# Kernel optimization log

Measured on AMD Instinct MI355X. Metric: run time of the kernel, lower is better.

## Reference

```python
import jax, jax.numpy as jnp
import numpy as np

B, M, NT, V, D, H, E, S = 4, 12, 12, 10000, 64, 3, 512, 32


def setup_inputs() -> dict:
    key = jax.random.key(0)
    ks = jax.random.split(key, 16)
    def rn(k, shape, scale=0.05):
        return jax.random.normal(k, shape, dtype=jnp.float32) * scale
    return {
        "tendency": jax.random.normal(ks[0], (B, M, V), dtype=jnp.float32),
        "periodicity": jax.random.normal(ks[1], (B, NT, V), dtype=jnp.float32),
        "edges": jax.random.randint(ks[2], (H, E, S), 0, V),
        "w1": rn(ks[3], (1, D)), "b1": rn(ks[4], (D,)),
        "w2": rn(ks[5], (D, D)), "b2": rn(ks[6], (D,)),
        "attn_w": rn(ks[7], (D, D)), "attn_a": rn(ks[8], (2 * D, 1)),
        "w_ih": rn(ks[9], (4 * D, D)), "w_hh": rn(ks[10], (4 * D, D)),
        "b_ih": rn(ks[11], (4 * D,)), "b_hh": rn(ks[12], (4 * D,)),
        "w_out": rn(ks[13], (2 * D, 1)), "b_out": rn(ks[14], (1,)),
    }


def _hypersage(X, edges, w, b):
    # X: (N, V, F); edges: (E, S) node indices. All edges have size S <= Q,
    # so torch's random subsampling is the identity.
    n, v, f = X.shape
    e, s = edges.shape
    gathered = X[:, edges, :]                      # (N, E, S, F)
    agg = gathered.mean(axis=2)                    # (N, E, F)
    flat = edges.reshape(-1)                       # (E*S,)
    contrib = jnp.broadcast_to(agg[:, :, None, :], (n, e, s, f)).reshape(n, e * s, f)
    X_out = jnp.zeros((n, v, f), X.dtype).at[:, flat, :].add(contrib)
    deg = jnp.zeros((v,), X.dtype).at[flat].add(1.0)
    deg = jnp.maximum(deg, 1.0)
    X_out = X_out / deg[None, :, None]
    return X_out @ w + b                           # Linear fc


def _attention(Xs, attn_w, attn_a):
    # Xs: (H, N, V, D)
    ref = Xs.mean(axis=0)                          # (N, V, D)
    wx = Xs @ attn_w                               # (H, N, V, D)
    wr = ref @ attn_w                              # (N, V, D)
    z = jnp.concatenate([wx, jnp.broadcast_to(wr[None], wx.shape)], axis=-1) @ attn_a
    z = jax.nn.leaky_relu(z, negative_slope=0.2)   # (H, N, V, 1)
    alpha = jax.nn.softmax(z, axis=0)
    return (alpha * Xs).sum(axis=0)                # (N, V, D)


def _lstm_final(x, w_ih, w_hh, b_ih, b_hh):
    # x: (BV, T, D) -> final hidden state (BV, D). PyTorch gate order i,f,g,o.
    bv, t, d = x.shape
    xg = x @ w_ih.T + (b_ih + b_hh)                # precompute input gates (BV, T, 4D)
    def step(carry, xg_t):
        h, c = carry
        g = xg_t + h @ w_hh.T
        i, f, gg, o = jnp.split(g, 4, axis=-1)
        c = jax.nn.sigmoid(f) * c + jax.nn.sigmoid(i) * jnp.tanh(gg)
        h = jax.nn.sigmoid(o) * jnp.tanh(c)
        return (h, c), None
    h0 = jnp.zeros((bv, d), x.dtype)
    (h, _), _ = jax.lax.scan(step, (h0, h0), jnp.swapaxes(xg, 0, 1))
    return h


def _branch(seq, edges, w1, b1, w2, b2, attn_w, attn_a, w_ih, w_hh, b_ih, b_hh):
    b, t, v = seq.shape
    X = seq.reshape(b * t, v, 1)                   # fold time into batch (same DAMHG per step)
    def per_hg(e):
        return _hypersage(_hypersage(X, e, w1, b1), e, w2, b2)
    xs = jax.vmap(per_hg)(edges)                   # (H, B*T, V, D)
    fused = _attention(xs, attn_w, attn_a)         # (B*T, V, D)
    d = fused.shape[-1]
    seq_v = fused.reshape(b, t, v, d).transpose(0, 2, 1, 3).reshape(b * v, t, d)
    h = _lstm_final(seq_v, w_ih, w_hh, b_ih, b_hh)
    return h.reshape(b, v, d)


def reference(tendency, periodicity, edges, w1, b1, w2, b2, attn_w, attn_a, w_ih, w_hh, b_ih, b_hh, w_out, b_out):
    h_t = _branch(tendency, edges, w1, b1, w2, b2, attn_w, attn_a, w_ih, w_hh, b_ih, b_hh)
    h_p = _branch(periodicity, edges, w1, b1, w2, b2, attn_w, attn_a, w_ih, w_hh, b_ih, b_hh)
    fusion = jnp.concatenate([h_t, h_p], axis=-1)  # (B, V, 2D)
    out = fusion @ w_out + b_out                   # (B, V, 1)
    return out[..., 0]
```

## Files before the change

### kernel.cpp

```cpp
#include <hip/hip_runtime.h>

#define NV 10000
#define NB 4
#define NTT 12
#define NSEQ 48
#define NH 3
#define NE 512
#define NS 32
#define ND 64
#define NVT 313

#define S_U   0
#define S_C1  64
#define S_V1  128
#define S_V2  192
#define S_SC  256
#define S_GU  272
#define S_GC  528
#define S_G0  784
#define F_INV 1040
#define F_M   (F_INV + NH*NV)
#define F_PQ  (F_M + NH*NV)
#define F_HT  (F_PQ + 4*NV*NSEQ)
#define I_CNT (F_HT + 2*NB*NV)
#define I_CUR (I_CNT + NH*NV)
#define I_OFF (I_CUR + NH*NV)
#define I_SLOT (I_OFF + NH*NV)
#define F_DYN (I_SLOT + NH*NE*NS)
#define XT_SZ  (NV*NSEQ)
#define AGG_SZ (NH*NE*NSEQ)
#define YZ_SZ  (NH*NV*NSEQ)

#define NZERO (2*NH*NV + NB*NV)

typedef __attribute__((ext_vector_type(8))) _Float16 f16x8;
typedef __attribute__((ext_vector_type(4))) float f32x4;

__device__ __forceinline__ unsigned short f2h(float x) {
  union { _Float16 h; unsigned short u; } c;
  c.h = (_Float16)x;
  return c.u;
}
__device__ __forceinline__ f16x8 ldsH(const unsigned short* p) {
  union { uint4 u; f16x8 v; } x;
  x.u = *(const uint4*)p;
  return x.v;
}

__global__ void k_init(const float* __restrict__ w1, const float* __restrict__ b1,
                       const float* __restrict__ w2, const float* __restrict__ b2,
                       const float* __restrict__ attn_w, const float* __restrict__ attn_a,
                       const float* __restrict__ w_ih, const float* __restrict__ b_ih,
                       const float* __restrict__ b_hh, float* __restrict__ ws,
                       int* __restrict__ cnt, float* __restrict__ out) {
  const int tid = threadIdx.x;
  if (blockIdx.x != 0) {
    const int g = (blockIdx.x - 1) * 256 + tid;
    if (g < 2 * NH * NV) cnt[g] = 0;
    else if (g < NZERO) out[g - 2 * NH * NV] = 0.0f;
    return;
  }
  __shared__ float u_s[64], c1_s[64];
  if (tid < 64) {
    float v1 = 0.f, v2 = 0.f, u = 0.f, c1 = 0.f;
    for (int d = 0; d < 64; ++d) {
      const float aw = attn_w[tid * 64 + d];
      v1 += aw * attn_a[d];
      v2 += aw * attn_a[64 + d];
      const float w2v = w2[d * 64 + tid];
      u  += w1[d] * w2v;
      c1 += b1[d] * w2v;
    }
    ws[S_U + tid] = u;  ws[S_C1 + tid] = c1;
    ws[S_V1 + tid] = v1; ws[S_V2 + tid] = v2;
    u_s[tid] = u; c1_s[tid] = c1;
  }
  __syncthreads();
  if (tid == 0) {
    float al = 0.f, be = 0.f, ga = 0.f, de = 0.f, ep = 0.f;
    for (int d = 0; d < 64; ++d) {
      const float v1 = ws[S_V1 + d], v2 = ws[S_V2 + d];
      al += u_s[d] * v1;  be += c1_s[d] * v1;
      ga += u_s[d] * v2;  de += c1_s[d] * v2;
      ep += b2[d] * (v1 + v2);
    }
    ws[S_SC + 0] = al; ws[S_SC + 1] = be; ws[S_SC + 2] = ga;
    ws[S_SC + 3] = de; ws[S_SC + 4] = ep;
  }
  {
    const int j = tid;
    float gu = 0.f, gc = 0.f, g0 = 0.f;
    for (int d = 0; d < 64; ++d) {
      const float w = w_ih[j * 64 + d];
      gu += w * u_s[d]; gc += w * c1_s[d]; g0 += w * b2[d];
    }
    ws[S_GU + j] = gu; ws[S_GC + j] = gc;
    ws[S_G0 + j] = g0 + b_ih[j] + b_hh[j];
  }
}

__global__ void k_count(const int* __restrict__ edges, int* __restrict__ counts) {
  const int g = blockIdx.x * 256 + threadIdx.x;
  if (g >= NH * NE * NS) return;
  const int h = g >> 14;
  atomicAdd(&counts[h * NV + edges[g]], 1);
}

__global__ void k_scan(const int* __restrict__ counts, int* __restrict__ offs,
                       float* __restrict__ invdeg, float* __restrict__ mvec) {
  const int h = blockIdx.x;
  const int tid = threadIdx.x;
  const int base = h * NV;
  const int CH = 10;
  int local[10];
  int run = 0;
  for (int i = 0; i < CH; ++i) {
    const int v = tid * CH + i;
    const int c = (v < NV) ? counts[base + v] : 0;
    local[i] = run; run += c;
  }
  __shared__ int sd[1024];
  sd[tid] = run;
  __syncthreads();
  int acc = run;
  for (int off = 1; off < 1024; off <<= 1) {
    const int t = (tid >= off) ? sd[tid - off] : 0;
    __syncthreads();
    acc += t; sd[tid] = acc;
    __syncthreads();
  }
  const int excl = acc - run;
  for (int i = 0; i < CH; ++i) {
    const int v = tid * CH + i;
    if (v < NV) {
      offs[base + v] = excl + local[i];
      const int c = counts[base + v];
      invdeg[base + v] = 1.0f / (float)((c > 0) ? c : 1);
      mvec[base + v] = (c > 0) ? 1.0f : 0.0f;
    }
  }
}

__global__ void k_fill(const int* __restrict__ edges, const int* __restrict__ offs,
                       int* __restrict__ cursor, int* __restrict__ slot_edge) {
  const int g = blockIdx.x * 256 + threadIdx.x;
  if (g >= NH * NE * NS) return;
  const int h = g >> 14;
  const int e = (g >> 5) & (NE - 1);
  const int v = edges[g];
  const int pos = atomicAdd(&cursor[h * NV + v], 1);
  slot_edge[h * NE * NS + offs[h * NV + v] + pos] = e;
}

__global__ void k_trans2(const float* __restrict__ s0, const float* __restrict__ s1,
                         float* __restrict__ xT, int xtS) {
  __shared__ float tile[128][49];
  const float* seq = blockIdx.y ? s1 : s0;
  float* o = xT + (size_t)blockIdx.y * xtS;
  const int v0 = blockIdx.x * 128;
  const int tid = threadIdx.x;
  for (int i = tid; i < 128 * NSEQ; i += 256) {
    const int n = i / 128, vl = i % 128;
    const int v = v0 + vl;
    tile[vl][n] = (v < NV) ? seq[n * NV + v] : 0.0f;
  }
  __syncthreads();
  for (int i = tid; i < 128 * NSEQ; i += 256) {
    const int vl = i / NSEQ, n = i % NSEQ;
    const int v = v0 + vl;
    if (v < NV) o[v * NSEQ + n] = tile[vl][n];
  }
}

__global__ void k_eagg1(const int* __restrict__ edges, const float* __restrict__ xT,
                        int xtS, float* __restrict__ agg, int aggS) {
  const int g = blockIdx.x * 256 + threadIdx.x;
  if (g >= NH * NE * 12 * 8) return;
  const float* x = xT + (size_t)blockIdx.y * xtS;
  float* a = agg + (size_t)blockIdx.y * aggS;
  const int sub = g & 7;
  const int o = g >> 3;
  const int n0 = (o % 12) * 4;
  const int e = (o / 12) % NE;
  const int h = o / (12 * NE);
  const int* ep = edges + (h * NE + e) * NS + sub * 4;
  float4 acc = make_float4(0.f, 0.f, 0.f, 0.f);
  #pragma unroll
  for (int s = 0; s < 4; ++s) {
    const float4 t = *(const float4*)&x[ep[s] * NSEQ + n0];
    acc.x += t.x; acc.y += t.y; acc.z += t.z; acc.w += t.w;
  }
  #pragma unroll
  for (int m = 1; m < 8; m <<= 1) {
    acc.x += __shfl_xor(acc.x, m);
    acc.y += __shfl_xor(acc.y, m);
    acc.z += __shfl_xor(acc.z, m);
    acc.w += __shfl_xor(acc.w, m);
  }
  if (sub == 0) {
    acc.x *= (1.0f / NS); acc.y *= (1.0f / NS); acc.z *= (1.0f / NS); acc.w *= (1.0f / NS);
    *(float4*)&a[(h * NE + e) * NSEQ + n0] = acc;
  }
}

__global__ void k_eagg2(const int* __restrict__ edges, const float* __restrict__ ysum,
                        int yS, const float* __restrict__ invdeg,
                        float* __restrict__ agg, int aggS) {
  const int g = blockIdx.x * 256 + threadIdx.x;
  if (g >= NH * NE * 12 * 8) return;
  const float* y = ysum + (size_t)blockIdx.y * yS;
  float* a = agg + (size_t)blockIdx.y * aggS;
  const int sub = g & 7;
  const int o = g >> 3;
  const int n0 = (o % 12) * 4;
  const int e = (o / 12) % NE;
  const int h = o / (12 * NE);
  const int* ep = edges + (h * NE + e) * NS + sub * 4;
  float4 acc = make_float4(0.f, 0.f, 0.f, 0.f);
  #pragma unroll
  for (int s = 0; s < 4; ++s) {
    const int v = ep[s];
    const float iv = invdeg[h * NV + v];
    const float4 t = *(const float4*)&y[(h * NV + v) * NSEQ + n0];
    acc.x += t.x * iv; acc.y += t.y * iv; acc.z += t.z * iv; acc.w += t.w * iv;
  }
  #pragma unroll
  for (int m = 1; m < 8; m <<= 1) {
    acc.x += __shfl_xor(acc.x, m);
    acc.y += __shfl_xor(acc.y, m);
    acc.z += __shfl_xor(acc.z, m);
    acc.w += __shfl_xor(acc.w, m);
  }
  if (sub == 0) {
    acc.x *= (1.0f / NS); acc.y *= (1.0f / NS); acc.z *= (1.0f / NS); acc.w *= (1.0f / NS);
    *(float4*)&a[(h * NE + e) * NSEQ + n0] = acc;
  }
}

__global__ void k_vg(const int* __restrict__ counts, const int* __restrict__ offs,
                     const int* __restrict__ slot_edge, const float* __restrict__ agg,
                     int aggS, float* __restrict__ outv, int outS) {
  const int g = blockIdx.x * 256 + threadIdx.x;
  if (g >= NH * NV * 12) return;
  const float* a = agg + (size_t)blockIdx.y * aggS;
  float* o = outv + (size_t)blockIdx.y * outS;
  const int n0 = (g % 12) * 4;
  const int v = (g / 12) % NV;
  const int h = g / (12 * NV);
  const int beg = offs[h * NV + v];
  const int cnt = counts[h * NV + v];
  const int* se = slot_edge + h * NE * NS;
  float4 acc = make_float4(0.f, 0.f, 0.f, 0.f);
  for (int i = 0; i < cnt; ++i) {
    const int e = se[beg + i];
    const float4 t = *(const float4*)&a[(h * NE + e) * NSEQ + n0];
    acc.x += t.x; acc.y += t.y; acc.z += t.z; acc.w += t.w;
  }
  *(float4*)&o[(h * NV + v) * NSEQ + n0] = acc;
}

__global__ void k_vgattn(const int* __restrict__ counts, const int* __restrict__ offs,
                         const int* __restrict__ slot_edge, const float* __restrict__ agg,
                         int aggS, const float* __restrict__ invdeg,
                         const float* __restrict__ mvec, const float* __restrict__ ws,
                         unsigned int* __restrict__ pq, int br0) {
  const int g = blockIdx.x * 256 + threadIdx.x;
  if (g >= NV * 12) return;
  const int bi = blockIdx.y;
  const float* a = agg + (size_t)bi * aggS;
  unsigned int* pbuf = pq + (size_t)(bi + br0) * NV * NSEQ;
  const int n0 = (g % 12) * 4;
  const int v = g / 12;
  const float al = ws[S_SC + 0], be = ws[S_SC + 1], ga = ws[S_SC + 2],
              de = ws[S_SC + 3], ep = ws[S_SC + 4];
  union { float4 v4; float f[4]; } zh[3];
  float mh[3];
  #pragma unroll
  for (int h = 0; h < NH; ++h) {
    const int beg = offs[h * NV + v];
    const int cnt = counts[h * NV + v];
    const int* se = slot_edge + h * NE * NS;
    float4 acc = make_float4(0.f, 0.f, 0.f, 0.f);
    for (int i = 0; i < cnt; ++i) {
      const int e = se[beg + i];
      const float4 t = *(const float4*)&a[(h * NE + e) * NSEQ + n0];
      acc.x += t.x; acc.y += t.y; acc.z += t.z; acc.w += t.w;
    }
    const float iv = invdeg[h * NV + v];
    zh[h].v4 = make_float4(acc.x * iv, acc.y * iv, acc.z * iv, acc.w * iv);
    mh[h] = mvec[h * NV + v];
  }
  const float mb = (mh[0] + mh[1] + mh[2]) * (1.f / 3.f);
  uint4 o4;
  unsigned int* op = (unsigned int*)&o4;
  #pragma unroll
  for (int j = 0; j < 4; ++j) {
    const float z0 = zh[0].f[j], z1 = zh[1].f[j], z2 = zh[2].f[j];
    const float zb = (z0 + z1 + z2) * (1.f / 3.f);
    float sc[3];
    const float zt[3] = {z0, z1, z2};
    #pragma unroll
    for (int h = 0; h < NH; ++h) {
      const float s = al * zt[h] + be * mh[h] + ga * zb + de * mb + ep;
      sc[h] = (s > 0.f) ? s : 0.2f * s;
    }
    const float mx = fmaxf(sc[0], fmaxf(sc[1], sc[2]));
    const float e0 = __expf(sc[0] - mx), e1 = __expf(sc[1] - mx), e2 = __expf(sc[2] - mx);
    const float inv = 1.0f / (e0 + e1 + e2);
    const float pv = (e0 * z0 + e1 * z1 + e2 * z2) * inv;
    const float qv = (e0 * mh[0] + e1 * mh[1] + e2 * mh[2]) * inv;
    op[j] = (unsigned int)f2h(pv) | ((unsigned int)f2h(qv) << 16);
  }
  *(uint4*)&pbuf[v * NSEQ + n0] = o4;
}

#define RS2 72
__launch_bounds__(256, 4)
__global__ void k_lstm2(const float* __restrict__ w_hh, const float* __restrict__ ws,
                        const unsigned int* __restrict__ pqbase,
                        const float* __restrict__ w_out, const float* __restrict__ b_out,
                        float* __restrict__ out) {
  __shared__ __align__(16) unsigned short smem[2 * 32 * RS2];
  __shared__ unsigned int pq_sh[NTT][32];
  const int tid = threadIdx.x;
  const int w = tid >> 6, lane = tid & 63, q = lane >> 4, l15 = lane & 15;
  const int bid = blockIdx.x;
  const int vt = bid % NVT;
  const int b  = (bid / NVT) % NB;
  const int br = bid / (NVT * NB);
  const int v0 = vt * 32;
  const int d = w * 16 + l15;

  union HU { uint4 u; f16x8 v; };

  const unsigned int* pqb = pqbase + (size_t)br * NV * NSEQ;
  if (tid < 96) {
    const int s = tid / 3, f4 = tid % 3;
    const int v = v0 + s;
    uint4 val = make_uint4(0u, 0u, 0u, 0u);
    if (v < NV) val = *(const uint4*)&pqb[v * NSEQ + b * NTT + f4 * 4];
    pq_sh[f4 * 4 + 0][s] = val.x; pq_sh[f4 * 4 + 1][s] = val.y;
    pq_sh[f4 * 4 + 2][s] = val.z; pq_sh[f4 * 4 + 3][s] = val.w;
  }

  f16x8 Bf[4][2];
  #pragma unroll
  for (int g = 0; g < 4; ++g)
    #pragma unroll
    for (int kh = 0; kh < 2; ++kh) {
      const float* wp = w_hh + (g * 64 + d) * 64 + kh * 32 + q * 8;
      const float4 lo = *(const float4*)wp;
      const float4 hi = *(const float4*)(wp + 4);
      HU f;
      f.u.x = (unsigned int)f2h(lo.x) | ((unsigned int)f2h(lo.y) << 16);
      f.u.y = (unsigned int)f2h(lo.z) | ((unsigned int)f2h(lo.w) << 16);
      f.u.z = (unsigned int)f2h(hi.x) | ((unsigned int)f2h(hi.y) << 16);
      f.u.w = (unsigned int)f2h(hi.z) | ((unsigned int)f2h(hi.w) << 16);
      Bf[g][kh] = f.v;
    }

  HU bex[4];
  #pragma unroll
  for (int g = 0; g < 4; ++g) {
    const float gu = ws[S_GU + g * 64 + d];
    const float gc = ws[S_GC + g * 64 + d];
    const float g0 = ws[S_G0 + g * 64 + d];
    bex[g].u.x = (q == 0) ? ((unsigned int)f2h(gu) | ((unsigned int)f2h(gc) << 16)) : 0u;
    bex[g].u.y = (q == 0) ? (unsigned int)f2h(g0) : 0u;
    bex[g].u.z = 0u; bex[g].u.w = 0u;
  }
  const float WO = w_out[br * 64 + d];
  const float BO = b_out[0];
  __syncthreads();

  f32x4 cst[2];
  float pr[2][4];
  #pragma unroll
  for (int mi = 0; mi < 2; ++mi) cst[mi] = (f32x4){0.f, 0.f, 0.f, 0.f};
  const f32x4 z4 = (f32x4){0.f, 0.f, 0.f, 0.f};

  #pragma unroll 1
  for (int t = 0; t < NTT; ++t) {
    const unsigned short* hr = smem + ((t + 1) & 1) * (32 * RS2);
    unsigned short* hw = smem + (t & 1) * (32 * RS2);
    const bool last = (t == NTT - 1);
    #pragma unroll
    for (int mi = 0; mi < 2; ++mi) {
      HU ae;
      ae.u.x = (q == 0) ? pq_sh[t][mi * 16 + l15] : 0u;
      ae.u.y = (q == 0) ? 0x3C00u : 0u;
      ae.u.z = 0u; ae.u.w = 0u;
      f32x4 aI = __builtin_amdgcn_mfma_f32_16x16x32_f16(ae.v, bex[0].v, z4, 0, 0, 0);
      f32x4 aF = __builtin_amdgcn_mfma_f32_16x16x32_f16(ae.v, bex[1].v, z4, 0, 0, 0);
      f32x4 aG = __builtin_amdgcn_mfma_f32_16x16x32_f16(ae.v, bex[2].v, z4, 0, 0, 0);
      f32x4 aO = __builtin_amdgcn_mfma_f32_16x16x32_f16(ae.v, bex[3].v, z4, 0, 0, 0);
      if (t > 0) {
        #pragma unroll
        for (int kh = 0; kh < 2; ++kh) {
          const f16x8 Ah = ldsH(&hr[(mi * 16 + l15) * RS2 + kh * 32 + q * 8]);
          aI = __builtin_amdgcn_mfma_f32_16x16x32_f16(Ah, Bf[0][kh], aI, 0, 0, 0);
          aF = __builtin_amdgcn_mfma_f32_16x16x32_f16(Ah, Bf[1][kh], aF, 0, 0, 0);
          aG = __builtin_amdgcn_mfma_f32_16x16x32_f16(Ah, Bf[2][kh], aG, 0, 0, 0);
          aO = __builtin_amdgcn_mfma_f32_16x16x32_f16(Ah, Bf[3][kh], aO, 0, 0, 0);
        }
      }
      #pragma unroll
      for (int r = 0; r < 4; ++r) {
        const float c  = cst[mi][r];
        const float ea = __expf(-aI[r]);
        const float eb = __expf(-2.0f * aG[r]);
        const float ef = __expf(-aF[r]);
        const float A  = 1.0f + ea, Bb = 1.0f + eb, Fd = 1.0f + ef;
        const float P  = A * Bb;
        const float numer = fmaf(c, P, (1.0f - eb) * Fd);
        const float cn = numer * __builtin_amdgcn_rcpf(Fd * P);
        cst[mi][r] = cn;
        const float ec = __expf(-aO[r]);
        const float ed = __expf(-2.0f * cn);
        const float h = (1.0f - ed) *
            __builtin_amdgcn_rcpf((1.0f + ec) * (1.0f + ed));
        if (!last) {
          hw[(mi * 16 + q * 4 + r) * RS2 + d] = f2h(h);
        } else {
          pr[mi][r] = h * WO;
        }
      }
    }
    __syncthreads();
  }
  float* fbuf = (float*)smem;
  #pragma unroll
  for (int mi = 0; mi < 2; ++mi)
    #pragma unroll
    for (int r = 0; r < 4; ++r) {
      float v = pr[mi][r];
      v += __shfl_xor(v, 1);
      v += __shfl_xor(v, 2);
      v += __shfl_xor(v, 4);
      v += __shfl_xor(v, 8);
      if (l15 == 0) fbuf[w * 32 + mi * 16 + q * 4 + r] = v;
    }
  __syncthreads();
  if (tid < 32) {
    const int v = v0 + tid;
    if (v < NV) {
      const float s = fbuf[tid] + fbuf[32 + tid] + fbuf[64 + tid] + fbuf[96 + tid];
      atomicAdd(&out[b * NV + v], s + ((br == 0) ? BO : 0.0f));
    }
  }
}

extern "C" void kernel_launch(void* const* d_in, const int* in_sizes, int n_in,
                              void* d_out, int out_size, void* d_ws, size_t ws_size,
                              hipStream_t stream) {
  const float* tend   = (const float*)d_in[0];
  const float* peri   = (const float*)d_in[1];
  const int*   edges  = (const int*)d_in[2];
  const float* w1     = (const float*)d_in[3];
  const float* b1     = (const float*)d_in[4];
  const float* w2     = (const float*)d_in[5];
  const float* b2     = (const float*)d_in[6];
  const float* attn_w = (const float*)d_in[7];
  const float* attn_a = (const float*)d_in[8];
  const float* w_ih   = (const float*)d_in[9];
  const float* w_hh   = (const float*)d_in[10];
  const float* b_ih   = (const float*)d_in[11];
  const float* b_hh   = (const float*)d_in[12];
  const float* w_out  = (const float*)d_in[13];
  const float* b_out  = (const float*)d_in[14];
  float* out = (float*)d_out;
  float* ws  = (float*)d_ws;
  int*   iws = (int*)d_ws;
  int* cnt = iws + I_CNT;
  int* cur = iws + I_CUR;
  int* off = iws + I_OFF;
  int* sed = iws + I_SLOT;
  unsigned int* pqw = (unsigned int*)(ws + F_PQ);

  const size_t need2 = ((size_t)F_DYN + 2 * (XT_SZ + AGG_SZ + YZ_SZ)) * 4;
  const bool batched = ws_size >= need2;
  const int nb = batched ? 2 : 1;
  float* XT  = ws + F_DYN;
  float* AGG = XT + (size_t)nb * XT_SZ;
  float* YZ  = AGG + (size_t)nb * AGG_SZ;

  k_init<<<1 + (NZERO + 255) / 256, 256, 0, stream>>>(
      w1, b1, w2, b2, attn_w, attn_a, w_ih, b_ih, b_hh, ws, cnt, out);
  k_count<<<(NH * NE * NS) / 256, 256, 0, stream>>>(edges, cnt);
  k_scan<<<NH, 1024, 0, stream>>>(cnt, off, ws + F_INV, ws + F_M);
  k_fill<<<(NH * NE * NS) / 256, 256, 0, stream>>>(edges, off, cur, sed);

  const int g_eagg = (NH * NE * 12 * 8) / 256;
  const int g_vg   = (NH * NV * 12 + 255) / 256;
  const int g_attn = (NV * 12 + 255) / 256;
  if (batched) {
    k_trans2<<<dim3((NV + 127) / 128, 2), 256, 0, stream>>>(tend, peri, XT, XT_SZ);
    k_eagg1<<<dim3(g_eagg, 2), 256, 0, stream>>>(edges, XT, XT_SZ, AGG, AGG_SZ);
    k_vg<<<dim3(g_vg, 2), 256, 0, stream>>>(cnt, off, sed, AGG, AGG_SZ, YZ, YZ_SZ);
    k_eagg2<<<dim3(g_eagg, 2), 256, 0, stream>>>(edges, YZ, YZ_SZ, ws + F_INV, AGG, AGG_SZ);
    k_vgattn<<<dim3(g_attn, 2), 256, 0, stream>>>(cnt, off, sed, AGG, AGG_SZ,
                                                  ws + F_INV, ws + F_M, ws, pqw, 0);
  } else {
    for (int br = 0; br < 2; ++br) {
      const float* seq = br ? peri : tend;
      k_trans2<<<dim3((NV + 127) / 128, 1), 256, 0, stream>>>(seq, seq, XT, 0);
      k_eagg1<<<dim3(g_eagg, 1), 256, 0, stream>>>(edges, XT, 0, AGG, 0);
      k_vg<<<dim3(g_vg, 1), 256, 0, stream>>>(cnt, off, sed, AGG, 0, YZ, 0);
      k_eagg2<<<dim3(g_eagg, 1), 256, 0, stream>>>(edges, YZ, 0, ws + F_INV, AGG, 0);
      k_vgattn<<<dim3(g_attn, 1), 256, 0, stream>>>(cnt, off, sed, AGG, 0,
                                                    ws + F_INV, ws + F_M, ws, pqw, br);
    }
  }
  k_lstm2<<<NVT * NB * 2, 256, 0, stream>>>(w_hh, ws, pqw, w_out, b_out, out);
}
```

Measured before the change: 238.1 us.

## Fold transpose into init kernel, fuse fill into scan, prescale tanh gate weights

Merges the input transpose into the init kernel's grid and moves the CSR slot fill into the scan kernel after a barrier. Together these remove two kernel launches from the preprocessing chain. The g-gate weights and biases of the LSTM are prescaled by -2 so the tanh exponent needs no per-step multiply. The LSTM launch bounds are raised to 8 blocks per CU. Doing the fill inside the scan runs it with only 3 blocks, which lowers parallelism, and the tighter launch bounds may cause register spills.

```diff
diff --git a/kernel.cpp b/kernel.cpp
--- a/kernel.cpp
+++ b/kernel.cpp
@@ -32,6 +32,8 @@
 #define YZ_SZ  (NH*NV*NSEQ)
 
 #define NZERO (2*NH*NV + NB*NV)
+#define ZBLK  ((NZERO + 255) / 256)
+#define TRB   ((NV + 127) / 128)
 
 typedef __attribute__((ext_vector_type(8))) _Float16 f16x8;
 typedef __attribute__((ext_vector_type(4))) float f32x4;
@@ -52,8 +54,30 @@
                        const float* __restrict__ attn_w, const float* __restrict__ attn_a,
                        const float* __restrict__ w_ih, const float* __restrict__ b_ih,
                        const float* __restrict__ b_hh, float* __restrict__ ws,
-                       int* __restrict__ cnt, float* __restrict__ out) {
+                       int* __restrict__ cnt, float* __restrict__ out,
+                       const float* __restrict__ s0, const float* __restrict__ s1,
+                       float* __restrict__ xT, int xtS) {
   const int tid = threadIdx.x;
+  if (blockIdx.x > ZBLK) {
+    __shared__ float tile[128][49];
+    const int bx = blockIdx.x - 1 - ZBLK;
+    const int brn = bx / TRB;
+    const int v0 = (bx % TRB) * 128;
+    const float* seq = brn ? s1 : s0;
+    float* o = xT + (size_t)brn * xtS;
+    for (int i = tid; i < 128 * NSEQ; i += 256) {
+      const int n = i / 128, vl = i % 128;
+      const int v = v0 + vl;
+      tile[vl][n] = (v < NV) ? seq[n * NV + v] : 0.0f;
+    }
+    __syncthreads();
+    for (int i = tid; i < 128 * NSEQ; i += 256) {
+      const int vl = i / NSEQ, n = i % NSEQ;
+      const int v = v0 + vl;
+      if (v < NV) o[v * NSEQ + n] = tile[vl][n];
+    }
+    return;
+  }
   if (blockIdx.x != 0) {
     const int g = (blockIdx.x - 1) * 256 + tid;
     if (g < 2 * NH * NV) cnt[g] = 0;
@@ -106,7 +130,9 @@
   atomicAdd(&counts[h * NV + edges[g]], 1);
 }
 
-__global__ void k_scan(const int* __restrict__ counts, int* __restrict__ offs,
+__global__ void k_scan(const int* __restrict__ edges, const int* __restrict__ counts,
+                       int* __restrict__ offs, int* __restrict__ cursor,
+                       int* __restrict__ slot_edge,
                        float* __restrict__ invdeg, float* __restrict__ mvec) {
   const int h = blockIdx.x;
   const int tid = threadIdx.x;
@@ -139,36 +165,12 @@
       mvec[base + v] = (c > 0) ? 1.0f : 0.0f;
     }
   }
-}
-
-__global__ void k_fill(const int* __restrict__ edges, const int* __restrict__ offs,
-                       int* __restrict__ cursor, int* __restrict__ slot_edge) {
-  const int g = blockIdx.x * 256 + threadIdx.x;
-  if (g >= NH * NE * NS) return;
-  const int h = g >> 14;
-  const int e = (g >> 5) & (NE - 1);
-  const int v = edges[g];
-  const int pos = atomicAdd(&cursor[h * NV + v], 1);
-  slot_edge[h * NE * NS + offs[h * NV + v] + pos] = e;
-}
-
-__global__ void k_trans2(const float* __restrict__ s0, const float* __restrict__ s1,
-                         float* __restrict__ xT, int xtS) {
-  __shared__ float tile[128][49];
-  const float* seq = blockIdx.y ? s1 : s0;
-  float* o = xT + (size_t)blockIdx.y * xtS;
-  const int v0 = blockIdx.x * 128;
-  const int tid = threadIdx.x;
-  for (int i = tid; i < 128 * NSEQ; i += 256) {
-    const int n = i / 128, vl = i % 128;
-    const int v = v0 + vl;
-    tile[vl][n] = (v < NV) ? seq[n * NV + v] : 0.0f;
-  }
   __syncthreads();
-  for (int i = tid; i < 128 * NSEQ; i += 256) {
-    const int vl = i / NSEQ, n = i % NSEQ;
-    const int v = v0 + vl;
-    if (v < NV) o[v * NSEQ + n] = tile[vl][n];
+  const int be = h * NE * NS;
+  for (int i = tid; i < NE * NS; i += 1024) {
+    const int v = edges[be + i];
+    const int pos = atomicAdd(&cursor[base + v], 1);
+    slot_edge[be + offs[base + v] + pos] = i >> 5;
   }
 }
 
@@ -315,7 +317,7 @@
 }
 
 #define RS2 72
-__launch_bounds__(256, 4)
+__launch_bounds__(256, 8)
 __global__ void k_lstm2(const float* __restrict__ w_hh, const float* __restrict__ ws,
                         const unsigned int* __restrict__ pqbase,
                         const float* __restrict__ w_out, const float* __restrict__ b_out,
@@ -345,26 +347,29 @@
 
   f16x8 Bf[4][2];
   #pragma unroll
-  for (int g = 0; g < 4; ++g)
+  for (int g = 0; g < 4; ++g) {
+    const float sc = (g == 2) ? -2.0f : 1.0f;
     #pragma unroll
     for (int kh = 0; kh < 2; ++kh) {
       const float* wp = w_hh + (g * 64 + d) * 64 + kh * 32 + q * 8;
       const float4 lo = *(const float4*)wp;
       const float4 hi = *(const float4*)(wp + 4);
       HU f;
-      f.u.x = (unsigned int)f2h(lo.x) | ((unsigned int)f2h(lo.y) << 16);
-      f.u.y = (unsigned int)f2h(lo.z) | ((unsigned int)f2h(lo.w) << 16);
-      f.u.z = (unsigned int)f2h(hi.x) | ((unsigned int)f2h(hi.y) << 16);
-      f.u.w = (unsigned int)f2h(hi.z) | ((unsigned int)f2h(hi.w) << 16);
+      f.u.x = (unsigned int)f2h(sc * lo.x) | ((unsigned int)f2h(sc * lo.y) << 16);
+      f.u.y = (unsigned int)f2h(sc * lo.z) | ((unsigned int)f2h(sc * lo.w) << 16);
+      f.u.z = (unsigned int)f2h(sc * hi.x) | ((unsigned int)f2h(sc * hi.y) << 16);
+      f.u.w = (unsigned int)f2h(sc * hi.z) | ((unsigned int)f2h(sc * hi.w) << 16);
       Bf[g][kh] = f.v;
     }
+  }
 
   HU bex[4];
   #pragma unroll
   for (int g = 0; g < 4; ++g) {
-    const float gu = ws[S_GU + g * 64 + d];
-    const float gc = ws[S_GC + g * 64 + d];
-    const float g0 = ws[S_G0 + g * 64 + d];
+    const float sc = (g == 2) ? -2.0f : 1.0f;
+    const float gu = sc * ws[S_GU + g * 64 + d];
+    const float gc = sc * ws[S_GC + g * 64 + d];
+    const float g0 = sc * ws[S_G0 + g * 64 + d];
     bex[g].u.x = (q == 0) ? ((unsigned int)f2h(gu) | ((unsigned int)f2h(gc) << 16)) : 0u;
     bex[g].u.y = (q == 0) ? (unsigned int)f2h(g0) : 0u;
     bex[g].u.z = 0u; bex[g].u.w = 0u;
@@ -408,7 +413,7 @@
       for (int r = 0; r < 4; ++r) {
         const float c  = cst[mi][r];
         const float ea = __expf(-aI[r]);
-        const float eb = __expf(-2.0f * aG[r]);
+        const float eb = __expf(aG[r]);
         const float ef = __expf(-aF[r]);
         const float A  = 1.0f + ea, Bb = 1.0f + eb, Fd = 1.0f + ef;
         const float P  = A * Bb;
@@ -447,6 +452,26 @@
       const float s = fbuf[tid] + fbuf[32 + tid] + fbuf[64 + tid] + fbuf[96 + tid];
       atomicAdd(&out[b * NV + v], s + ((br == 0) ? BO : 0.0f));
     }
+  }
+}
+
+__global__ void k_trans2(const float* __restrict__ s0, const float* __restrict__ s1,
+                         float* __restrict__ xT, int xtS) {
+  __shared__ float tile[128][49];
+  const float* seq = blockIdx.y ? s1 : s0;
+  float* o = xT + (size_t)blockIdx.y * xtS;
+  const int v0 = blockIdx.x * 128;
+  const int tid = threadIdx.x;
+  for (int i = tid; i < 128 * NSEQ; i += 256) {
+    const int n = i / 128, vl = i % 128;
+    const int v = v0 + vl;
+    tile[vl][n] = (v < NV) ? seq[n * NV + v] : 0.0f;
+  }
+  __syncthreads();
+  for (int i = tid; i < 128 * NSEQ; i += 256) {
+    const int vl = i / NSEQ, n = i % NSEQ;
+    const int v = v0 + vl;
+    if (v < NV) o[v * NSEQ + n] = tile[vl][n];
   }
 }
 
@@ -484,17 +509,17 @@
   float* AGG = XT + (size_t)nb * XT_SZ;
   float* YZ  = AGG + (size_t)nb * AGG_SZ;
 
-  k_init<<<1 + (NZERO + 255) / 256, 256, 0, stream>>>(
-      w1, b1, w2, b2, attn_w, attn_a, w_ih, b_ih, b_hh, ws, cnt, out);
+  const int initg = batched ? (1 + ZBLK + 2 * TRB) : (1 + ZBLK);
+  k_init<<<initg, 256, 0, stream>>>(
+      w1, b1, w2, b2, attn_w, attn_a, w_ih, b_ih, b_hh, ws, cnt, out,
+      tend, peri, XT, XT_SZ);
   k_count<<<(NH * NE * NS) / 256, 256, 0, stream>>>(edges, cnt);
-  k_scan<<<NH, 1024, 0, stream>>>(cnt, off, ws + F_INV, ws + F_M);
-  k_fill<<<(NH * NE * NS) / 256, 256, 0, stream>>>(edges, off, cur, sed);
+  k_scan<<<NH, 1024, 0, stream>>>(edges, cnt, off, cur, sed, ws + F_INV, ws + F_M);
 
   const int g_eagg = (NH * NE * 12 * 8) / 256;
   const int g_vg   = (NH * NV * 12 + 255) / 256;
   const int g_attn = (NV * 12 + 255) / 256;
   if (batched) {
-    k_trans2<<<dim3((NV + 127) / 128, 2), 256, 0, stream>>>(tend, peri, XT, XT_SZ);
     k_eagg1<<<dim3(g_eagg, 2), 256, 0, stream>>>(edges, XT, XT_SZ, AGG, AGG_SZ);
     k_vg<<<dim3(g_vg, 2), 256, 0, stream>>>(cnt, off, sed, AGG, AGG_SZ, YZ, YZ_SZ);
     k_eagg2<<<dim3(g_eagg, 2), 256, 0, stream>>>(edges, YZ, YZ_SZ, ws + F_INV, AGG, AGG_SZ);
@@ -503,7 +528,7 @@
   } else {
     for (int br = 0; br < 2; ++br) {
       const float* seq = br ? peri : tend;
-      k_trans2<<<dim3((NV + 127) / 128, 1), 256, 0, stream>>>(seq, seq, XT, 0);
+      k_trans2<<<dim3(TRB, 1), 256, 0, stream>>>(seq, seq, XT, 0);
       k_eagg1<<<dim3(g_eagg, 1), 256, 0, stream>>>(edges, XT, 0, AGG, 0);
       k_vg<<<dim3(g_vg, 1), 256, 0, stream>>>(cnt, off, sed, AGG, 0, YZ, 0);
       k_eagg2<<<dim3(g_eagg, 1), 256, 0, stream>>>(edges, YZ, 0, ws + F_INV, AGG, 0);
```

Result: slower. 444.2 us (+86.6%).
